# Performance work log

Hardware: AMD Instinct MI355X
Metric: run time of the kernel (lower is better)

Reference implementation:

```python
import jax, jax.numpy as jnp
import numpy as np

N_NODES = 100000
N_EDGES = 1600000
F_IN, HIDDEN, N_CLASS = 256, 64, 2


def _gcn_conv(x, W, b, src, dst, norm, n):
    # PyG GCNConv: linear (no bias) -> normalized scatter-add -> bias
    h = x @ W                                  # [N, out]
    msg = h[src] * norm[:, None]               # gather + scale, [E+N, out]
    agg = jax.ops.segment_sum(msg, dst, num_segments=n)
    return agg + b


def setup_inputs() -> dict:
    key = jax.random.key(0)
    ks = jax.random.split(key, 8)
    x = jax.random.normal(ks[0], (N_NODES, F_IN), dtype=jnp.float32)
    edge_index = jax.random.randint(ks[1], (2, N_EDGES), 0, N_NODES, dtype=jnp.int32)
    W1 = jax.random.normal(ks[2], (F_IN, HIDDEN), dtype=jnp.float32) / np.sqrt(F_IN).astype(np.float32)
    b1 = jnp.zeros((HIDDEN,), dtype=jnp.float32)
    W2 = jax.random.normal(ks[3], (HIDDEN, HIDDEN), dtype=jnp.float32) / np.sqrt(HIDDEN).astype(np.float32)
    b2 = jnp.zeros((HIDDEN,), dtype=jnp.float32)
    W3 = jax.random.normal(ks[4], (HIDDEN, N_CLASS), dtype=jnp.float32) / np.sqrt(HIDDEN).astype(np.float32)
    b3 = jnp.zeros((N_CLASS,), dtype=jnp.float32)
    return {"x": x, "edge_index": edge_index, "W1": W1, "b1": b1, "W2": W2, "b2": b2, "W3": W3, "b3": b3}


def reference(x, edge_index, W1, b1, W2, b2, W3, b3):
    n = x.shape[0]
    # add self-loops (GCNConv default)
    loops = jnp.arange(n, dtype=edge_index.dtype)
    src = jnp.concatenate([edge_index[0], loops])
    dst = jnp.concatenate([edge_index[1], loops])
    # symmetric normalization D^-1/2 A_hat D^-1/2
    deg = jax.ops.segment_sum(jnp.ones_like(src, dtype=x.dtype), dst, num_segments=n)
    deg_inv_sqrt = jnp.where(deg > 0, jax.lax.rsqrt(jnp.maximum(deg, 1.0)), 0.0)
    norm = deg_inv_sqrt[src] * deg_inv_sqrt[dst]
    # layer 1 + relu (dropout is identity in eval mode)
    h = jax.nn.relu(_gcn_conv(x, W1, b1, src, dst, norm, n))
    # layer 2 + relu
    h = jax.nn.relu(_gcn_conv(h, W2, b2, src, dst, norm, n))
    # output layer + log_softmax
    h = _gcn_conv(h, W3, b3, src, dst, norm, n)
    return jax.nn.log_softmax(h, axis=1)
```

## Files before the change

kernel.cpp:

```cpp
#include <hip/hip_runtime.h>
#include <math.h>

#define F_IN 256
#define HID  64
#define BSH  8
#define BSPAN 256
#define CHUNK 16384
#define NBK_MAX 512

typedef __bf16 bf16x8 __attribute__((ext_vector_type(8)));
typedef float  floatx4 __attribute__((ext_vector_type(4)));

__global__ __launch_bounds__(256) void k_hist(const int* __restrict__ dst,
                                              int* __restrict__ cntT,
                                              int E, int NCH, int NBK) {
    __shared__ int hist[NBK_MAX];
    int t = threadIdx.x, c = blockIdx.x;
    hist[t] = 0; hist[t + 256] = 0;
    __syncthreads();
    int base = c * CHUNK;
#pragma unroll 4
    for (int j = 0; j < CHUNK / 256; j++) {
        int e = base + j * 256 + t;
        if (e < E) atomicAdd(&hist[dst[e] >> BSH], 1);
    }
    __syncthreads();
    for (int b = t; b < NBK; b += 256) cntT[b * NCH + c] = hist[b];
}

__global__ __launch_bounds__(256) void k_scanA(const int* __restrict__ cntT,
                                               int* __restrict__ off,
                                               int* __restrict__ partials, int S) {
    __shared__ int sh[256];
    int tid = threadIdx.x;
    int base = blockIdx.x * 1024 + tid * 4;
    int v[4];
    int s = 0;
#pragma unroll
    for (int j = 0; j < 4; j++) {
        int idx = base + j;
        v[j] = (idx < S) ? cntT[idx] : 0;
        s += v[j];
    }
    sh[tid] = s;
    __syncthreads();
    int mysum = s;
    for (int o = 1; o < 256; o <<= 1) {
        int tv = (tid >= o) ? sh[tid - o] : 0;
        __syncthreads();
        sh[tid] += tv;
        __syncthreads();
    }
    int pref = sh[tid] - mysum;
#pragma unroll
    for (int j = 0; j < 4; j++) {
        int idx = base + j;
        if (idx < S) off[idx] = pref;
        pref += v[j];
    }
    if (tid == 255) partials[blockIdx.x] = sh[255];
}

__global__ void k_scanB(int* __restrict__ partials, int* __restrict__ off,
                        int nblk, int S) {
    if (blockIdx.x == 0 && threadIdx.x == 0) {
        int run = 0;
        for (int b = 0; b < nblk; b++) { int t = partials[b]; partials[b] = run; run += t; }
        off[S] = run;
    }
}

__global__ void k_scanC(int* __restrict__ off, const int* __restrict__ partials, int S) {
    int i = blockIdx.x * blockDim.x + threadIdx.x;
    if (i < S) off[i] += partials[i >> 10];
}

__global__ __launch_bounds__(256) void k_sortwrite(const int* __restrict__ src,
                                                   const int* __restrict__ dst,
                                                   const int* __restrict__ off,
                                                   int* __restrict__ ebuf,
                                                   int E, int NCH, int NBK) {
    __shared__ int cur[NBK_MAX];
    int t = threadIdx.x, c = blockIdx.x;
    for (int b = t; b < NBK; b += 256) cur[b] = off[b * NCH + c];
    __syncthreads();
    int base = c * CHUNK;
#pragma unroll 4
    for (int j = 0; j < CHUNK / 256; j++) {
        int e = base + j * 256 + t;
        if (e < E) {
            int s = src[e];
            int d = dst[e];
            int pos = atomicAdd(&cur[d >> BSH], 1);
            ebuf[pos] = (s << BSH) | (d & (BSPAN - 1));
        }
    }
}

__global__ __launch_bounds__(256) void k_bucket_csr(const int* __restrict__ off,
                                                    const int* __restrict__ ebuf,
                                                    int* __restrict__ rp,
                                                    float* __restrict__ dinv,
                                                    int* __restrict__ esrc,
                                                    int N, int NCH, int NBK) {
    __shared__ int cnt[BSPAN];
    __shared__ int sh[BSPAN];
    int b = blockIdx.x, t = threadIdx.x;
    int base = off[b * NCH];
    int end  = off[(b + 1) * NCH];

    cnt[t] = 0;
    __syncthreads();
    for (int i = base + t; i < end; i += 256) atomicAdd(&cnt[ebuf[i] & (BSPAN - 1)], 1);
    __syncthreads();

    int c = cnt[t];
    sh[t] = c;
    __syncthreads();
    for (int o = 1; o < 256; o <<= 1) {
        int tv = (t >= o) ? sh[t - o] : 0;
        __syncthreads();
        sh[t] += tv;
        __syncthreads();
    }
    int excl = sh[t] - c;

    int node = (b << BSH) + t;
    if (node < N) {
        rp[node] = base + excl;
        dinv[node] = rsqrtf((float)(1 + c));
    }
    if (b == NBK - 1 && t == 0) rp[N] = end;
    __syncthreads();

    cnt[t] = base + excl;
    __syncthreads();
    for (int i = base + t; i < end; i += 256) {
        int v = ebuf[i];
        int p = atomicAdd(&cnt[v & (BSPAN - 1)], 1);
        esrc[p] = v >> BSH;
    }
}

__global__ __launch_bounds__(256) void k_prepw(const float* __restrict__ W1,
                                               __bf16* __restrict__ w1h, __bf16* __restrict__ w1l,
                                               const float* __restrict__ W2,
                                               __bf16* __restrict__ w2h, __bf16* __restrict__ w2l) {
    int t = threadIdx.x + blockIdx.x * blockDim.x;
    for (int idx = t; idx < 64 * 256; idx += 256 * 8) {
        int c = idx >> 8, k = idx & 255;
        float w = W1[k * 64 + c];
        __bf16 h = (__bf16)w;
        w1h[idx] = h;
        w1l[idx] = (__bf16)(w - (float)h);
    }
    for (int idx = t; idx < 64 * 64; idx += 256 * 8) {
        int c = idx >> 6, k = idx & 63;
        float w = W2[k * 64 + c];
        __bf16 h = (__bf16)w;
        w2h[idx] = h;
        w2l[idx] = (__bf16)(w - (float)h);
    }
}

template <int K>
__global__ __launch_bounds__(256) void k_gemm_mfma(const float* __restrict__ A,
                                                   const __bf16* __restrict__ BtH,
                                                   const __bf16* __restrict__ BtL,
                                                   const float* __restrict__ dinv,
                                                   float* __restrict__ C, int nrows) {
    int wave = threadIdx.x >> 6;
    int lane = threadIdx.x & 63;
    int m = lane & 15;
    int q = lane >> 4;
    int row0 = blockIdx.x * 64 + wave * 16;
    int arow = row0 + m;
    bool rvalid = arow < nrows;
    const float* ap = A + (size_t)arow * K + q * 8;

    floatx4 acc[4] = {{0.f, 0.f, 0.f, 0.f}, {0.f, 0.f, 0.f, 0.f},
                      {0.f, 0.f, 0.f, 0.f}, {0.f, 0.f, 0.f, 0.f}};

    for (int k0 = 0; k0 < K; k0 += 32) {
        float4 f0 = make_float4(0.f, 0.f, 0.f, 0.f);
        float4 f1 = make_float4(0.f, 0.f, 0.f, 0.f);
        if (rvalid) {
            f0 = *(const float4*)(ap + k0);
            f1 = *(const float4*)(ap + k0 + 4);
        }
        float af[8] = {f0.x, f0.y, f0.z, f0.w, f1.x, f1.y, f1.z, f1.w};
        bf16x8 ah, al;
#pragma unroll
        for (int j = 0; j < 8; j++) {
            __bf16 h = (__bf16)af[j];
            ah[j] = h;
            al[j] = (__bf16)(af[j] - (float)h);
        }
#pragma unroll
        for (int c = 0; c < 4; c++) {
            const __bf16* bp = BtH + (size_t)(c * 16 + m) * K + k0 + q * 8;
            const __bf16* bq = BtL + (size_t)(c * 16 + m) * K + k0 + q * 8;
            bf16x8 bh = *(const bf16x8*)bp;
            bf16x8 bl = *(const bf16x8*)bq;
            acc[c] = __builtin_amdgcn_mfma_f32_16x16x32_bf16(ah, bh, acc[c], 0, 0, 0);
            acc[c] = __builtin_amdgcn_mfma_f32_16x16x32_bf16(al, bh, acc[c], 0, 0, 0);
            acc[c] = __builtin_amdgcn_mfma_f32_16x16x32_bf16(ah, bl, acc[c], 0, 0, 0);
        }
    }

#pragma unroll
    for (int i = 0; i < 4; i++) {
        int r = row0 + q * 4 + i;
        if (r < nrows) {
            float di = dinv[r];
#pragma unroll
            for (int c = 0; c < 4; c++)
                C[(size_t)r * 64 + c * 16 + m] = acc[c][i] * di;
        }
    }
}

template <int MODE>
__global__ __launch_bounds__(256) void k_agg64(const float* __restrict__ hs,
                                               const float* __restrict__ dinv,
                                               const int* __restrict__ rp,
                                               const int* __restrict__ esrc,
                                               const float* __restrict__ bias,
                                               const float* __restrict__ W3,
                                               float* __restrict__ out, int n) {
    int lane = threadIdx.x & 63;
    int nid = blockIdx.x * 4 + (threadIdx.x >> 6);
    if (nid >= n) return;
    nid = __builtin_amdgcn_readfirstlane(nid);

    float dii = dinv[nid];
    int e0 = rp[nid];
    int e1 = rp[nid + 1];

    float a0 = hs[(size_t)nid * 64 + lane];
    float a1 = 0.f, a2 = 0.f, a3 = 0.f, a4 = 0.f, a5 = 0.f, a6 = 0.f, a7 = 0.f;

    for (int e = e0; e < e1; e += 8) {
        int last = e1 - 1;
        int i0 = esrc[e];
        int i1 = esrc[min(e + 1, last)];
        int i2 = esrc[min(e + 2, last)];
        int i3 = esrc[min(e + 3, last)];
        int i4 = esrc[min(e + 4, last)];
        int i5 = esrc[min(e + 5, last)];
        int i6 = esrc[min(e + 6, last)];
        int i7 = esrc[min(e + 7, last)];
        float v0 = hs[(size_t)i0 * 64 + lane];
        float v1 = hs[(size_t)i1 * 64 + lane];
        float v2 = hs[(size_t)i2 * 64 + lane];
        float v3 = hs[(size_t)i3 * 64 + lane];
        float v4 = hs[(size_t)i4 * 64 + lane];
        float v5 = hs[(size_t)i5 * 64 + lane];
        float v6 = hs[(size_t)i6 * 64 + lane];
        float v7 = hs[(size_t)i7 * 64 + lane];
        a0 += v0;
        a1 += (e + 1 <= last) ? v1 : 0.f;
        a2 += (e + 2 <= last) ? v2 : 0.f;
        a3 += (e + 3 <= last) ? v3 : 0.f;
        a4 += (e + 4 <= last) ? v4 : 0.f;
        a5 += (e + 5 <= last) ? v5 : 0.f;
        a6 += (e + 6 <= last) ? v6 : 0.f;
        a7 += (e + 7 <= last) ? v7 : 0.f;
    }

    float acc = ((a0 + a1) + (a2 + a3)) + ((a4 + a5) + (a6 + a7));
    acc = acc * dii + bias[lane];
    acc = fmaxf(acc, 0.f);

    if (MODE == 0) {
        out[(size_t)nid * 64 + lane] = acc;
    } else {
        float2 w3 = ((const float2*)W3)[lane];
        float p0 = acc * w3.x;
        float p1 = acc * w3.y;
#pragma unroll
        for (int o = 32; o > 0; o >>= 1) {
            p0 += __shfl_xor(p0, o, 64);
            p1 += __shfl_xor(p1, o, 64);
        }
        if (lane == 0) ((float2*)out)[nid] = make_float2(p0 * dii, p1 * dii);
    }
}

__global__ __launch_bounds__(256) void k_final(const float2* __restrict__ h3s,
                                               const float* __restrict__ dinv,
                                               const int* __restrict__ rp,
                                               const int* __restrict__ esrc,
                                               const float* __restrict__ b3,
                                               float* __restrict__ out, int n) {
    int i = blockIdx.x * blockDim.x + threadIdx.x;
    if (i >= n) return;
    float dii = dinv[i];
    float2 h = h3s[i];
    float ax = h.x, ay = h.y;
    float bx = 0.f, by = 0.f, cx = 0.f, cy = 0.f, dx = 0.f, dy = 0.f;
    int e0 = rp[i], e1 = rp[i + 1];
    for (int e = e0; e < e1; e += 4) {
        int last = e1 - 1;
        int s0 = esrc[e];
        int s1 = esrc[min(e + 1, last)];
        int s2 = esrc[min(e + 2, last)];
        int s3 = esrc[min(e + 3, last)];
        float2 v0 = h3s[s0];
        float2 v1 = h3s[s1];
        float2 v2 = h3s[s2];
        float2 v3 = h3s[s3];
        ax += v0.x; ay += v0.y;
        bx += (e + 1 <= last) ? v1.x : 0.f; by += (e + 1 <= last) ? v1.y : 0.f;
        cx += (e + 2 <= last) ? v2.x : 0.f; cy += (e + 2 <= last) ? v2.y : 0.f;
        dx += (e + 3 <= last) ? v3.x : 0.f; dy += (e + 3 <= last) ? v3.y : 0.f;
    }
    float l0 = ((ax + bx) + (cx + dx)) * dii + b3[0];
    float l1 = ((ay + by) + (cy + dy)) * dii + b3[1];
    float m = fmaxf(l0, l1);
    float lse = m + logf(expf(l0 - m) + expf(l1 - m));
    ((float2*)out)[i] = make_float2(l0 - lse, l1 - lse);
}

extern "C" void kernel_launch(void* const* d_in, const int* in_sizes, int n_in,
                              void* d_out, int out_size, void* d_ws, size_t ws_size,
                              hipStream_t stream) {
    const float* x   = (const float*)d_in[0];
    const int*   ei  = (const int*)d_in[1];
    const float* W1  = (const float*)d_in[2];
    const float* b1  = (const float*)d_in[3];
    const float* W2  = (const float*)d_in[4];
    const float* b2  = (const float*)d_in[5];
    const float* W3  = (const float*)d_in[6];
    const float* b3  = (const float*)d_in[7];
    float* out = (float*)d_out;

    const int N = in_sizes[0] / F_IN;
    const int E = in_sizes[1] / 2;
    const int* src = ei;
    const int* dst = ei + E;

    const int NBK = (N + BSPAN - 1) / BSPAN;
    const int NCH = (E + CHUNK - 1) / CHUNK;
    const int S   = NBK * NCH;

    char* p = (char*)d_ws;
    auto alloc = [&](size_t bytes) -> void* {
        void* r = (void*)p;
        p += (bytes + 255) & ~(size_t)255;
        return r;
    };
    int*    cntT     = (int*)alloc((size_t)S * 4);
    int*    off      = (int*)alloc((size_t)(S + 1) * 4);
    int*    partials = (int*)alloc(4096);
    int*    ebuf     = (int*)alloc((size_t)E * 4);
    int*    esrc     = (int*)alloc((size_t)E * 4);
    int*    rp       = (int*)alloc((size_t)(N + 1) * 4);
    float*  dinv     = (float*)alloc((size_t)N * 4);
    float*  bufA     = (float*)alloc((size_t)N * HID * 4);
    float*  bufB     = (float*)alloc((size_t)N * HID * 4);
    float*  h3       = (float*)alloc((size_t)N * 2 * 4);
    __bf16* w1h      = (__bf16*)alloc(64 * 256 * 2);
    __bf16* w1l      = (__bf16*)alloc(64 * 256 * 2);
    __bf16* w2h      = (__bf16*)alloc(64 * 64 * 2);
    __bf16* w2l      = (__bf16*)alloc(64 * 64 * 2);

    const int T = 256;
    int scanBlocks = (S + 1023) / 1024;

    k_prepw<<<8, T, 0, stream>>>(W1, w1h, w1l, W2, w2h, w2l);

    k_hist<<<NCH, T, 0, stream>>>(dst, cntT, E, NCH, NBK);
    k_scanA<<<scanBlocks, T, 0, stream>>>(cntT, off, partials, S);
    k_scanB<<<1, 64, 0, stream>>>(partials, off, scanBlocks, S);
    k_scanC<<<(S + T - 1) / T, T, 0, stream>>>(off, partials, S);
    k_sortwrite<<<NCH, T, 0, stream>>>(src, dst, off, ebuf, E, NCH, NBK);
    k_bucket_csr<<<NBK, T, 0, stream>>>(off, ebuf, rp, dinv, esrc, N, NCH, NBK);

    int gemmBlocks = (N + 63) / 64;
    k_gemm_mfma<F_IN><<<gemmBlocks, T, 0, stream>>>(x, w1h, w1l, dinv, bufA, N);
    k_agg64<0><<<(N + 3) / 4, T, 0, stream>>>(bufA, dinv, rp, esrc, b1, nullptr, bufB, N);

    k_gemm_mfma<HID><<<gemmBlocks, T, 0, stream>>>(bufB, w2h, w2l, dinv, bufA, N);
    k_agg64<1><<<(N + 3) / 4, T, 0, stream>>>(bufA, dinv, rp, esrc, b2, W3, h3, N);

    k_final<<<(N + T - 1) / T, T, 0, stream>>>((const float2*)h3, dinv, rp, esrc, b3, out, N);
}
```

Measured before the change: 449.7 us.

## Stage GEMM A tiles through LDS with async loads and pre-fragment weights

The MFMA GEMM now loads A rows into double-buffered shared memory using global_load_lds direct-to-LDS copies, with a rotated segment layout so that per-lane reads avoid bank conflicts. The next chunk is prefetched while the current one is computed. The weight split (bf16 hi/lo) is also pre-arranged into per-lane MFMA fragment order, so each B load is a contiguous 16-byte read per lane. This targets the uncoalesced strided A reads and scattered B reads of the old kernel, at the cost of LDS use and a barrier per chunk.

```diff
diff --git a/kernel.cpp b/kernel.cpp
--- a/kernel.cpp
+++ b/kernel.cpp
@@ -143,74 +143,98 @@
 }
 
 __global__ __launch_bounds__(256) void k_prepw(const float* __restrict__ W1,
-                                               __bf16* __restrict__ w1h, __bf16* __restrict__ w1l,
+                                               __bf16* __restrict__ f1h, __bf16* __restrict__ f1l,
                                                const float* __restrict__ W2,
-                                               __bf16* __restrict__ w2h, __bf16* __restrict__ w2l) {
+                                               __bf16* __restrict__ f2h, __bf16* __restrict__ f2l) {
     int t = threadIdx.x + blockIdx.x * blockDim.x;
-    for (int idx = t; idx < 64 * 256; idx += 256 * 8) {
-        int c = idx >> 8, k = idx & 255;
-        float w = W1[k * 64 + c];
+    for (int idx = t; idx < 16384; idx += 2048) {
+        int j = idx & 7, lane = (idx >> 3) & 63, ch2 = (idx >> 9) & 7, c = idx >> 12;
+        int k = ch2 * 32 + (lane >> 4) * 8 + j, col = c * 16 + (lane & 15);
+        float w = W1[k * 64 + col];
         __bf16 h = (__bf16)w;
-        w1h[idx] = h;
-        w1l[idx] = (__bf16)(w - (float)h);
-    }
-    for (int idx = t; idx < 64 * 64; idx += 256 * 8) {
-        int c = idx >> 6, k = idx & 63;
-        float w = W2[k * 64 + c];
+        f1h[idx] = h; f1l[idx] = (__bf16)(w - (float)h);
+    }
+    for (int idx = t; idx < 4096; idx += 2048) {
+        int j = idx & 7, lane = (idx >> 3) & 63, ch2 = (idx >> 9) & 1, c = idx >> 10;
+        int k = ch2 * 32 + (lane >> 4) * 8 + j, col = c * 16 + (lane & 15);
+        float w = W2[k * 64 + col];
         __bf16 h = (__bf16)w;
-        w2h[idx] = h;
-        w2l[idx] = (__bf16)(w - (float)h);
+        f2h[idx] = h; f2l[idx] = (__bf16)(w - (float)h);
     }
 }
 
 template <int K>
 __global__ __launch_bounds__(256) void k_gemm_mfma(const float* __restrict__ A,
-                                                   const __bf16* __restrict__ BtH,
-                                                   const __bf16* __restrict__ BtL,
+                                                   const __bf16* __restrict__ BfH,
+                                                   const __bf16* __restrict__ BfL,
                                                    const float* __restrict__ dinv,
                                                    float* __restrict__ C, int nrows) {
-    int wave = threadIdx.x >> 6;
-    int lane = threadIdx.x & 63;
-    int m = lane & 15;
-    int q = lane >> 4;
-    int row0 = blockIdx.x * 64 + wave * 16;
-    int arow = row0 + m;
-    bool rvalid = arow < nrows;
-    const float* ap = A + (size_t)arow * K + q * 8;
+    constexpr int KC = 64;
+    constexpr int NCHK = K / KC;
+    constexpr int NCH32 = K / 32;
+    __shared__ float As[2][64 * KC];
+
+    const int t = threadIdx.x;
+    const int wave = t >> 6, lane = t & 63;
+    const int m = lane & 15, q = lane >> 4;
+    const int row0 = blockIdx.x * 64;
+
+    const int s_sub = lane >> 4;
+    const int s_seg = lane & 15;
+
+    auto stage = [&](int ch, int buf) {
+#pragma unroll
+        for (int j = 0; j < 4; j++) {
+            int lr = wave * 16 + j * 4 + s_sub;
+            int gr = row0 + lr; if (gr > nrows - 1) gr = nrows - 1;
+            int gs = (s_seg - lr) & 15;
+            const float* g = A + (size_t)gr * K + ch * KC + gs * 4;
+            float* l = &As[buf][(size_t)lr * KC + s_seg * 4];
+            __builtin_amdgcn_global_load_lds(
+                (const __attribute__((address_space(1))) void*)g,
+                (__attribute__((address_space(3))) void*)l, 16, 0, 0);
+        }
+    };
 
     floatx4 acc[4] = {{0.f, 0.f, 0.f, 0.f}, {0.f, 0.f, 0.f, 0.f},
                       {0.f, 0.f, 0.f, 0.f}, {0.f, 0.f, 0.f, 0.f}};
 
-    for (int k0 = 0; k0 < K; k0 += 32) {
-        float4 f0 = make_float4(0.f, 0.f, 0.f, 0.f);
-        float4 f1 = make_float4(0.f, 0.f, 0.f, 0.f);
-        if (rvalid) {
-            f0 = *(const float4*)(ap + k0);
-            f1 = *(const float4*)(ap + k0 + 4);
+    stage(0, 0);
+    __syncthreads();
+
+    for (int ch = 0; ch < NCHK; ch++) {
+        if (ch + 1 < NCHK) stage(ch + 1, (ch + 1) & 1);
+
+        const float* arow = &As[ch & 1][(size_t)(wave * 16 + m) * KC];
+#pragma unroll
+        for (int jj = 0; jj < 2; jj++) {
+            int ch2 = ch * 2 + jj;
+            int s0 = jj * 8 + q * 2;
+            float4 v0 = *(const float4*)(arow + (((s0 + m) & 15) * 4));
+            float4 v1 = *(const float4*)(arow + (((s0 + 1 + m) & 15) * 4));
+            float af[8] = {v0.x, v0.y, v0.z, v0.w, v1.x, v1.y, v1.z, v1.w};
+            bf16x8 ah, al;
+#pragma unroll
+            for (int j = 0; j < 8; j++) {
+                __bf16 h = (__bf16)af[j];
+                ah[j] = h;
+                al[j] = (__bf16)(af[j] - (float)h);
+            }
+#pragma unroll
+            for (int c = 0; c < 4; c++) {
+                const bf16x8 bh = *(const bf16x8*)(BfH + ((size_t)(c * NCH32 + ch2) * 64 + lane) * 8);
+                const bf16x8 bl = *(const bf16x8*)(BfL + ((size_t)(c * NCH32 + ch2) * 64 + lane) * 8);
+                acc[c] = __builtin_amdgcn_mfma_f32_16x16x32_bf16(ah, bh, acc[c], 0, 0, 0);
+                acc[c] = __builtin_amdgcn_mfma_f32_16x16x32_bf16(al, bh, acc[c], 0, 0, 0);
+                acc[c] = __builtin_amdgcn_mfma_f32_16x16x32_bf16(ah, bl, acc[c], 0, 0, 0);
+            }
         }
-        float af[8] = {f0.x, f0.y, f0.z, f0.w, f1.x, f1.y, f1.z, f1.w};
-        bf16x8 ah, al;
-#pragma unroll
-        for (int j = 0; j < 8; j++) {
-            __bf16 h = (__bf16)af[j];
-            ah[j] = h;
-            al[j] = (__bf16)(af[j] - (float)h);
-        }
-#pragma unroll
-        for (int c = 0; c < 4; c++) {
-            const __bf16* bp = BtH + (size_t)(c * 16 + m) * K + k0 + q * 8;
-            const __bf16* bq = BtL + (size_t)(c * 16 + m) * K + k0 + q * 8;
-            bf16x8 bh = *(const bf16x8*)bp;
-            bf16x8 bl = *(const bf16x8*)bq;
-            acc[c] = __builtin_amdgcn_mfma_f32_16x16x32_bf16(ah, bh, acc[c], 0, 0, 0);
-            acc[c] = __builtin_amdgcn_mfma_f32_16x16x32_bf16(al, bh, acc[c], 0, 0, 0);
-            acc[c] = __builtin_amdgcn_mfma_f32_16x16x32_bf16(ah, bl, acc[c], 0, 0, 0);
-        }
+        __syncthreads();
     }
 
 #pragma unroll
     for (int i = 0; i < 4; i++) {
-        int r = row0 + q * 4 + i;
+        int r = row0 + wave * 16 + q * 4 + i;
         if (r < nrows) {
             float di = dinv[r];
 #pragma unroll
@@ -360,15 +384,15 @@
     float*  bufA     = (float*)alloc((size_t)N * HID * 4);
     float*  bufB     = (float*)alloc((size_t)N * HID * 4);
     float*  h3       = (float*)alloc((size_t)N * 2 * 4);
-    __bf16* w1h      = (__bf16*)alloc(64 * 256 * 2);
-    __bf16* w1l      = (__bf16*)alloc(64 * 256 * 2);
-    __bf16* w2h      = (__bf16*)alloc(64 * 64 * 2);
-    __bf16* w2l      = (__bf16*)alloc(64 * 64 * 2);
+    __bf16* f1h      = (__bf16*)alloc(16384 * 2);
+    __bf16* f1l      = (__bf16*)alloc(16384 * 2);
+    __bf16* f2h      = (__bf16*)alloc(4096 * 2);
+    __bf16* f2l      = (__bf16*)alloc(4096 * 2);
 
     const int T = 256;
     int scanBlocks = (S + 1023) / 1024;
 
-    k_prepw<<<8, T, 0, stream>>>(W1, w1h, w1l, W2, w2h, w2l);
+    k_prepw<<<8, T, 0, stream>>>(W1, f1h, f1l, W2, f2h, f2l);
 
     k_hist<<<NCH, T, 0, stream>>>(dst, cntT, E, NCH, NBK);
     k_scanA<<<scanBlocks, T, 0, stream>>>(cntT, off, partials, S);
@@ -378,10 +402,10 @@
     k_bucket_csr<<<NBK, T, 0, stream>>>(off, ebuf, rp, dinv, esrc, N, NCH, NBK);
 
     int gemmBlocks = (N + 63) / 64;
-    k_gemm_mfma<F_IN><<<gemmBlocks, T, 0, stream>>>(x, w1h, w1l, dinv, bufA, N);
+    k_gemm_mfma<F_IN><<<gemmBlocks, T, 0, stream>>>(x, f1h, f1l, dinv, bufA, N);
     k_agg64<0><<<(N + 3) / 4, T, 0, stream>>>(bufA, dinv, rp, esrc, b1, nullptr, bufB, N);
 
-    k_gemm_mfma<HID><<<gemmBlocks, T, 0, stream>>>(bufB, w2h, w2l, dinv, bufA, N);
+    k_gemm_mfma<HID><<<gemmBlocks, T, 0, stream>>>(bufB, f2h, f2l, dinv, bufA, N);
     k_agg64<1><<<(N + 3) / 4, T, 0, stream>>>(bufA, dinv, rp, esrc, b2, W3, h3, N);
 
     k_final<<<(N + T - 1) / T, T, 0, stream>>>((const float2*)h3, dinv, rp, esrc, b3, out, N);
```

New measurement: 414.9 us. 1.08x faster.
